# Kernel optimization log

Hardware: AMD Instinct MI355X
Metric: run time of the kernel (lower is better)

Reference implementation:

```python
import math
import jax, jax.numpy as jnp
import numpy as np

N = 100000
E_RAND = 800000
IN_F, HID, OUT_F, HEADS = 128, 64, 64, 4
NOISE_SCALE = 1.0 * math.sqrt(2.0 * math.log(1.25 / 0.05))  # dp_rate=1, eps=1, del=0.05


def setup_inputs() -> dict:
    key = jax.random.key(0)
    ks = jax.random.split(key, 12)
    x = jax.random.normal(ks[0], (N, IN_F), dtype=jnp.float32)
    src_r = jax.random.randint(ks[1], (E_RAND,), 0, N, dtype=jnp.int32)
    dst_r = jax.random.randint(ks[2], (E_RAND,), 0, N, dtype=jnp.int32)
    loops = jnp.arange(N, dtype=jnp.int32)  # add_self_loop
    src = jnp.concatenate([src_r, loops])
    dst = jnp.concatenate([dst_r, loops])
    # layer 0: GATConv(in=128, out=64, heads=4)
    s0 = 1.0 / math.sqrt(IN_F)
    W0 = jax.random.normal(ks[3], (IN_F, HEADS * HID), dtype=jnp.float32) * s0
    al0 = jax.random.normal(ks[4], (HEADS, HID), dtype=jnp.float32) * 0.1
    ar0 = jax.random.normal(ks[5], (HEADS, HID), dtype=jnp.float32) * 0.1
    b0 = jnp.zeros((HEADS * HID,), dtype=jnp.float32)
    # layer 1: GATConv(in=256, out=64, heads=1)
    s1 = 1.0 / math.sqrt(HEADS * HID)
    W1 = jax.random.normal(ks[6], (HEADS * HID, OUT_F), dtype=jnp.float32) * s1
    al1 = jax.random.normal(ks[7], (1, OUT_F), dtype=jnp.float32) * 0.1
    ar1 = jax.random.normal(ks[8], (1, OUT_F), dtype=jnp.float32) * 0.1
    b1 = jnp.zeros((OUT_F,), dtype=jnp.float32)
    # DP gaussian noise added after first GAT layer (torch.normal(0,1,x.shape))
    noise = jax.random.normal(ks[9], (N, HEADS * HID), dtype=jnp.float32)
    return {"x": x, "src": src, "dst": dst, "W0": W0, "al0": al0, "ar0": ar0,
            "b0": b0, "W1": W1, "al1": al1, "ar1": ar1, "b1": b1, "noise": noise}


def gat_conv(x, src, dst, W, al, ar, b, apply_act):
    """DGL GATConv: per-edge attention, edge softmax over dst, scatter-sum."""
    H, D = al.shape
    h = (x @ W).reshape(-1, H, D)                      # [N,H,D]
    el = jnp.sum(h * al, axis=-1)                      # [N,H]
    er = jnp.sum(h * ar, axis=-1)                      # [N,H]
    e = jax.nn.leaky_relu(el[src] + er[dst], 0.2)      # [E,H]
    emax = jax.ops.segment_max(e, dst, num_segments=N) # [N,H]
    a = jnp.exp(e - emax[dst])
    denom = jax.ops.segment_sum(a, dst, num_segments=N)
    alpha = a / denom[dst]                             # [E,H] edge softmax
    msg = h[src] * alpha[:, :, None]                   # [E,H,D]
    out = jax.ops.segment_sum(msg, dst, num_segments=N) + b.reshape(1, H, D)
    if apply_act:
        out = jax.nn.leaky_relu(out, 0.01)             # F.leaky_relu default slope
    return out.reshape(-1, H * D)                      # flatten(1)


def reference(x, src, dst, W0, al0, ar0, b0, W1, al1, ar1, b1, noise):
    h = gat_conv(x, src, dst, W0, al0, ar0, b0, apply_act=True)   # [N, 256]
    h = h + NOISE_SCALE * noise                                   # DP noise after layer 0
    out = gat_conv(h, src, dst, W1, al1, ar1, b1, apply_act=False)  # [N, 64]
    return out
```

## Files before the change

kernel.cpp:

```cpp
#include <hip/hip_runtime.h>
#include <hip/hip_bf16.h>
#include <math.h>

#define IN_F 128
#define HID 64
#define HEADS 4
#define HD0 (HEADS * HID)
#define OUT_F 64
#define NOISE_SCALE 2.5372725354060904f

typedef __bf16 bf16x8 __attribute__((ext_vector_type(8)));
typedef float f32x4 __attribute__((ext_vector_type(4)));

__device__ __forceinline__ float bf2f(unsigned short u) {
    return __uint_as_float(((unsigned)u) << 16);
}
__device__ __forceinline__ unsigned short f2bf(float f) {
    unsigned u = __float_as_uint(f);
    u = u + 0x7fffu + ((u >> 16) & 1u);
    return (unsigned short)(u >> 16);
}

__global__ __launch_bounds__(256) void cast_bf16_kernel(
    const float* __restrict__ in, unsigned short* __restrict__ out, size_t n8) {
    size_t i = (size_t)blockIdx.x * 256 + threadIdx.x;
    if (i >= n8) return;
    const float4 a = ((const float4*)in)[i * 2];
    const float4 b = ((const float4*)in)[i * 2 + 1];
    ushort4 o0, o1;
    o0.x = f2bf(a.x); o0.y = f2bf(a.y); o0.z = f2bf(a.z); o0.w = f2bf(a.w);
    o1.x = f2bf(b.x); o1.y = f2bf(b.y); o1.z = f2bf(b.z); o1.w = f2bf(b.w);
    ((ushort4*)out)[i * 2] = o0;
    ((ushort4*)out)[i * 2 + 1] = o1;
}

__global__ __launch_bounds__(256) void tcast_kernel(
    const float* __restrict__ W, unsigned short* __restrict__ Wt, int K, int NC) {
    int i = blockIdx.x * 256 + threadIdx.x;
    if (i >= K * NC) return;
    int n = i / K, k = i % K;
    Wt[n * K + k] = f2bf(W[(size_t)k * NC + n]);
}

template <int K, int H>
__global__ __launch_bounds__(256) void gemm_fused_kernel(
    const unsigned short* __restrict__ A, const unsigned short* __restrict__ Bt,
    unsigned short* __restrict__ C, const float* __restrict__ al,
    const float* __restrict__ ar, float* __restrict__ el,
    float* __restrict__ er, int M, int NC) {
    constexpr int BSTR = K + 8;
    constexpr int ASTR = 40;
    __shared__ __align__(16) unsigned short Bs[64 * BSTR];
    __shared__ __align__(16) unsigned short As[128 * ASTR];
    const int tid = threadIdx.x;
    const int lane = tid & 63, w = tid >> 6;
    const int row0 = blockIdx.y * 128;
    const int n0 = blockIdx.x * 64;
    for (int i = tid; i < 64 * (K / 8); i += 256) {
        int n = i / (K / 8), kc = i % (K / 8);
        *(uint4*)(Bs + n * BSTR + kc * 8) =
            *(const uint4*)(Bt + (size_t)(n0 + n) * K + kc * 8);
    }
    f32x4 acc[2][4] = {};
    const int q = lane >> 4, c = lane & 15;
    const int r_st = tid >> 1, hh = tid & 1;
    for (int k0 = 0; k0 < K; k0 += 32) {
        int gr = row0 + r_st;
        uint4 av0 = make_uint4(0, 0, 0, 0), av1 = make_uint4(0, 0, 0, 0);
        if (gr < M) {
            const unsigned short* ap = A + (size_t)gr * K + k0 + hh * 16;
            av0 = *(const uint4*)(ap);
            av1 = *(const uint4*)(ap + 8);
        }
        __syncthreads();
        *(uint4*)(As + r_st * ASTR + hh * 16) = av0;
        *(uint4*)(As + r_st * ASTR + hh * 16 + 8) = av1;
        __syncthreads();
        bf16x8 af[2], bfr[4];
        af[0] = *(const bf16x8*)(As + (w * 32 + c) * ASTR + q * 8);
        af[1] = *(const bf16x8*)(As + (w * 32 + 16 + c) * ASTR + q * 8);
#pragma unroll
        for (int nt = 0; nt < 4; ++nt)
            bfr[nt] = *(const bf16x8*)(Bs + (nt * 16 + c) * BSTR + k0 + q * 8);
#pragma unroll
        for (int mt = 0; mt < 2; ++mt)
#pragma unroll
            for (int nt = 0; nt < 4; ++nt)
                acc[mt][nt] = __builtin_amdgcn_mfma_f32_16x16x32_bf16(
                    af[mt], bfr[nt], acc[mt][nt], 0, 0, 0);
    }
    float alv[4], arv[4];
#pragma unroll
    for (int nt = 0; nt < 4; ++nt) {
        alv[nt] = al[n0 + nt * 16 + c];
        arv[nt] = ar[n0 + nt * 16 + c];
    }
    const int head = n0 >> 6;
#pragma unroll
    for (int mt = 0; mt < 2; ++mt) {
#pragma unroll
        for (int r = 0; r < 4; ++r) {
            int grow = row0 + w * 32 + mt * 16 + q * 4 + r;
            bool ok = grow < M;
            float elp = 0.f, erp = 0.f;
#pragma unroll
            for (int nt = 0; nt < 4; ++nt) {
                float v = acc[mt][nt][r];
                elp += v * alv[nt];
                erp += v * arv[nt];
                if (ok) C[(size_t)grow * NC + n0 + nt * 16 + c] = f2bf(v);
            }
#pragma unroll
            for (int o = 8; o > 0; o >>= 1) {
                elp += __shfl_down(elp, o, 16);
                erp += __shfl_down(erp, o, 16);
            }
            if (c == 0 && ok) {
                el[(size_t)grow * H + head] = elp;
                er[(size_t)grow * H + head] = erp;
            }
        }
    }
}

__global__ __launch_bounds__(256) void degree_kernel(
    const int* __restrict__ dst, int* __restrict__ deg, int E) {
    int e = blockIdx.x * 256 + threadIdx.x;
    if (e < E) atomicAdd(&deg[dst[e]], 1);
}

__global__ __launch_bounds__(256) void scan_block_kernel(
    const int* __restrict__ deg, int* __restrict__ off,
    int* __restrict__ bsum, int N) {
    __shared__ int s[256];
    int i = blockIdx.x * 256 + threadIdx.x;
    int v = (i < N) ? deg[i] : 0;
    s[threadIdx.x] = v;
    __syncthreads();
    for (int d = 1; d < 256; d <<= 1) {
        int t = (threadIdx.x >= d) ? s[threadIdx.x - d] : 0;
        __syncthreads();
        s[threadIdx.x] += t;
        __syncthreads();
    }
    if (i < N) off[i] = s[threadIdx.x] - v;
    if (threadIdx.x == 255) bsum[blockIdx.x] = s[255];
}

__global__ __launch_bounds__(512) void scan_partials_kernel(int* __restrict__ bsum, int nb) {
    __shared__ int s[512];
    int v = (threadIdx.x < nb) ? bsum[threadIdx.x] : 0;
    s[threadIdx.x] = v;
    __syncthreads();
    for (int d = 1; d < 512; d <<= 1) {
        int t = (threadIdx.x >= d) ? s[threadIdx.x - d] : 0;
        __syncthreads();
        s[threadIdx.x] += t;
        __syncthreads();
    }
    if (threadIdx.x < nb) bsum[threadIdx.x] = s[threadIdx.x] - v;
}

__global__ __launch_bounds__(256) void add_offsets_kernel(
    int* __restrict__ off, int* __restrict__ cur,
    const int* __restrict__ bsum, int N, int E) {
    int i = blockIdx.x * 256 + threadIdx.x;
    if (i < N) {
        int v = off[i] + bsum[blockIdx.x];
        off[i] = v;
        cur[i] = v;
    }
    if (i == 0) off[N] = E;
}

__global__ __launch_bounds__(256) void fill_csr_kernel(
    const int* __restrict__ src, const int* __restrict__ dst,
    int* __restrict__ cur, int* __restrict__ csr_src, int E) {
    int e = blockIdx.x * 256 + threadIdx.x;
    if (e >= E) return;
    int d = dst[e];
    int pos = atomicAdd(&cur[d], 1);
    csr_src[pos] = src[e];
}

__global__ __launch_bounds__(256) void agg0_kernel(
    const int* __restrict__ off, const int* __restrict__ csr_src,
    const unsigned short* __restrict__ h,
    const float* __restrict__ el,
    const float* __restrict__ er,
    const float* __restrict__ b0, const float* __restrict__ noise,
    unsigned short* __restrict__ out, int N) {
    int gt = blockIdx.x * 256 + threadIdx.x;
    int n = gt >> 6;
    int lane = gt & 63;
    if (n >= N) return;
    int hd = lane >> 4;
    float ern = er[(size_t)n * 4 + hd];
    int beg = off[n], end = off[n + 1];
    float ax = 0.f, ay = 0.f, az = 0.f, aw = 0.f, l = 0.f;
    int p = beg;
    for (; p + 4 <= end; p += 4) {
        int s0 = csr_src[p], s1 = csr_src[p + 1];
        int s2 = csr_src[p + 2], s3 = csr_src[p + 3];
        float e0 = el[(size_t)s0 * 4 + hd];
        float e1 = el[(size_t)s1 * 4 + hd];
        float e2 = el[(size_t)s2 * 4 + hd];
        float e3 = el[(size_t)s3 * 4 + hd];
        ushort4 u0 = *(const ushort4*)(h + (size_t)s0 * HD0 + lane * 4);
        ushort4 u1 = *(const ushort4*)(h + (size_t)s1 * HD0 + lane * 4);
        ushort4 u2 = *(const ushort4*)(h + (size_t)s2 * HD0 + lane * 4);
        ushort4 u3 = *(const ushort4*)(h + (size_t)s3 * HD0 + lane * 4);
        e0 += ern; e1 += ern; e2 += ern; e3 += ern;
        e0 = e0 > 0.f ? e0 : 0.2f * e0;
        e1 = e1 > 0.f ? e1 : 0.2f * e1;
        e2 = e2 > 0.f ? e2 : 0.2f * e2;
        e3 = e3 > 0.f ? e3 : 0.2f * e3;
        float w0 = __expf(e0), w1 = __expf(e1), w2 = __expf(e2), w3 = __expf(e3);
        ax += w0 * bf2f(u0.x) + w1 * bf2f(u1.x) + w2 * bf2f(u2.x) + w3 * bf2f(u3.x);
        ay += w0 * bf2f(u0.y) + w1 * bf2f(u1.y) + w2 * bf2f(u2.y) + w3 * bf2f(u3.y);
        az += w0 * bf2f(u0.z) + w1 * bf2f(u1.z) + w2 * bf2f(u2.z) + w3 * bf2f(u3.z);
        aw += w0 * bf2f(u0.w) + w1 * bf2f(u1.w) + w2 * bf2f(u2.w) + w3 * bf2f(u3.w);
        l += (w0 + w1) + (w2 + w3);
    }
    for (; p < end; ++p) {
        int s0 = csr_src[p];
        float e0 = el[(size_t)s0 * 4 + hd] + ern;
        e0 = e0 > 0.f ? e0 : 0.2f * e0;
        float w0 = __expf(e0);
        ushort4 u0 = *(const ushort4*)(h + (size_t)s0 * HD0 + lane * 4);
        ax += w0 * bf2f(u0.x);
        ay += w0 * bf2f(u0.y);
        az += w0 * bf2f(u0.z);
        aw += w0 * bf2f(u0.w);
        l += w0;
    }
    float rd = 1.f / l;
    const float4 bv = *(const float4*)(b0 + lane * 4);
    const float4 nv = *(const float4*)(noise + (size_t)n * HD0 + lane * 4);
    float ox = ax * rd + bv.x; ox = ox > 0.f ? ox : 0.01f * ox; ox += NOISE_SCALE * nv.x;
    float oy = ay * rd + bv.y; oy = oy > 0.f ? oy : 0.01f * oy; oy += NOISE_SCALE * nv.y;
    float oz = az * rd + bv.z; oz = oz > 0.f ? oz : 0.01f * oz; oz += NOISE_SCALE * nv.z;
    float ow = aw * rd + bv.w; ow = ow > 0.f ? ow : 0.01f * ow; ow += NOISE_SCALE * nv.w;
    ushort4 o;
    o.x = f2bf(ox); o.y = f2bf(oy); o.z = f2bf(oz); o.w = f2bf(ow);
    *(ushort4*)(out + (size_t)n * HD0 + lane * 4) = o;
}

__global__ __launch_bounds__(256) void agg1_kernel(
    const int* __restrict__ off, const int* __restrict__ csr_src,
    const unsigned short* __restrict__ h,
    const float* __restrict__ el,
    const float* __restrict__ er,
    const float* __restrict__ b1, float* __restrict__ out, int N) {
    int gt = blockIdx.x * 256 + threadIdx.x;
    int n = gt >> 6;
    int lane = gt & 63;
    if (n >= N) return;
    float ern = er[n];
    int beg = off[n], end = off[n + 1];
    float acc = 0.f, l = 0.f;
    int p = beg;
    for (; p + 4 <= end; p += 4) {
        int s0 = csr_src[p], s1 = csr_src[p + 1];
        int s2 = csr_src[p + 2], s3 = csr_src[p + 3];
        float e0 = el[s0], e1 = el[s1], e2 = el[s2], e3 = el[s3];
        float v0 = bf2f(h[(size_t)s0 * 64 + lane]);
        float v1 = bf2f(h[(size_t)s1 * 64 + lane]);
        float v2 = bf2f(h[(size_t)s2 * 64 + lane]);
        float v3 = bf2f(h[(size_t)s3 * 64 + lane]);
        e0 += ern; e1 += ern; e2 += ern; e3 += ern;
        e0 = e0 > 0.f ? e0 : 0.2f * e0;
        e1 = e1 > 0.f ? e1 : 0.2f * e1;
        e2 = e2 > 0.f ? e2 : 0.2f * e2;
        e3 = e3 > 0.f ? e3 : 0.2f * e3;
        float w0 = __expf(e0), w1 = __expf(e1), w2 = __expf(e2), w3 = __expf(e3);
        acc += w0 * v0 + w1 * v1 + w2 * v2 + w3 * v3;
        l += (w0 + w1) + (w2 + w3);
    }
    for (; p < end; ++p) {
        int s0 = csr_src[p];
        float e0 = el[s0] + ern;
        e0 = e0 > 0.f ? e0 : 0.2f * e0;
        float w0 = __expf(e0);
        acc += w0 * bf2f(h[(size_t)s0 * 64 + lane]);
        l += w0;
    }
    out[(size_t)n * 64 + lane] = acc / l + b1[lane];
}

extern "C" void kernel_launch(void* const* d_in, const int* in_sizes, int n_in,
                              void* d_out, int out_size, void* d_ws, size_t ws_size,
                              hipStream_t stream) {
    const float* x     = (const float*)d_in[0];
    const int*   src   = (const int*)d_in[1];
    const int*   dst   = (const int*)d_in[2];
    const float* W0    = (const float*)d_in[3];
    const float* al0   = (const float*)d_in[4];
    const float* ar0   = (const float*)d_in[5];
    const float* b0    = (const float*)d_in[6];
    const float* W1    = (const float*)d_in[7];
    const float* al1   = (const float*)d_in[8];
    const float* ar1   = (const float*)d_in[9];
    const float* b1    = (const float*)d_in[10];
    const float* noise = (const float*)d_in[11];

    const int N = in_sizes[0] / IN_F;
    const int E = in_sizes[1];
    const int NB = (N + 255) / 256;

    char* p = (char*)d_ws;
    unsigned short* x_bf   = (unsigned short*)p; p += (size_t)N * IN_F * 2;
    unsigned short* h0     = (unsigned short*)p; p += (size_t)N * HD0 * 2;
    unsigned short* agg0b  = (unsigned short*)p; p += (size_t)N * HD0 * 2;
    unsigned short* h1     = (unsigned short*)p; p += (size_t)N * OUT_F * 2;
    unsigned short* W0t    = (unsigned short*)p; p += (size_t)IN_F * HD0 * 2;
    unsigned short* W1t    = (unsigned short*)p; p += (size_t)HD0 * OUT_F * 2;
    float* el     = (float*)p; p += (size_t)N * HEADS * 4;
    float* er     = (float*)p; p += (size_t)N * HEADS * 4;
    int* deg    = (int*)p; p += (size_t)N * 4;
    int* cur    = (int*)p; p += (size_t)N * 4;
    int* off    = (int*)p; p += ((size_t)N + 4) * 4;
    int* bsum   = (int*)p; p += 512 * 4;
    int* csr_src= (int*)p; p += (size_t)E * 4;

    {
        size_t n8 = (size_t)N * IN_F / 8;
        cast_bf16_kernel<<<(unsigned)((n8 + 255) / 256), 256, 0, stream>>>(x, x_bf, n8);
    }
    tcast_kernel<<<(IN_F * HD0 + 255) / 256, 256, 0, stream>>>(W0, W0t, IN_F, HD0);
    tcast_kernel<<<(HD0 * OUT_F + 255) / 256, 256, 0, stream>>>(W1, W1t, HD0, OUT_F);

    hipMemsetAsync(deg, 0, (size_t)N * sizeof(int), stream);
    degree_kernel<<<(E + 255) / 256, 256, 0, stream>>>(dst, deg, E);
    scan_block_kernel<<<NB, 256, 0, stream>>>(deg, off, bsum, N);
    scan_partials_kernel<<<1, 512, 0, stream>>>(bsum, NB);
    add_offsets_kernel<<<NB, 256, 0, stream>>>(off, cur, bsum, N, E);
    fill_csr_kernel<<<(E + 255) / 256, 256, 0, stream>>>(src, dst, cur, csr_src, E);

    const int MB = (N + 127) / 128;

    {
        dim3 grid(HD0 / 64, MB);
        gemm_fused_kernel<IN_F, HEADS><<<grid, 256, 0, stream>>>(
            x_bf, W0t, h0, al0, ar0, el, er, N, HD0);
    }
    agg0_kernel<<<(N * 64 + 255) / 256, 256, 0, stream>>>(
        off, csr_src, h0, el, er, b0, noise, agg0b, N);

    {
        dim3 grid(OUT_F / 64, MB);
        gemm_fused_kernel<HD0, 1><<<grid, 256, 0, stream>>>(
            agg0b, W1t, h1, al1, ar1, el, er, N, OUT_F);
    }
    agg1_kernel<<<(N * 64 + 255) / 256, 256, 0, stream>>>(
        off, csr_src, h1, el, er, b1, (float*)d_out, N);
}
```

Measured before the change: 483.4 us.

## Widen per-lane gather vectors in aggregation kernels and fuse setup launches

```diff
diff --git a/kernel.cpp b/kernel.cpp
--- a/kernel.cpp
+++ b/kernel.cpp
@@ -21,9 +21,22 @@
     return (unsigned short)(u >> 16);
 }
 
+__device__ __forceinline__ void acc8(float* acc, const uint4& u, float wt) {
+    acc[0] += wt * __uint_as_float(u.x << 16);
+    acc[1] += wt * __uint_as_float(u.x & 0xffff0000u);
+    acc[2] += wt * __uint_as_float(u.y << 16);
+    acc[3] += wt * __uint_as_float(u.y & 0xffff0000u);
+    acc[4] += wt * __uint_as_float(u.z << 16);
+    acc[5] += wt * __uint_as_float(u.z & 0xffff0000u);
+    acc[6] += wt * __uint_as_float(u.w << 16);
+    acc[7] += wt * __uint_as_float(u.w & 0xffff0000u);
+}
+
 __global__ __launch_bounds__(256) void cast_bf16_kernel(
-    const float* __restrict__ in, unsigned short* __restrict__ out, size_t n8) {
+    const float* __restrict__ in, unsigned short* __restrict__ out, size_t n8,
+    int* __restrict__ deg, int N) {
     size_t i = (size_t)blockIdx.x * 256 + threadIdx.x;
+    if (i < (size_t)N) deg[i] = 0;
     if (i >= n8) return;
     const float4 a = ((const float4*)in)[i * 2];
     const float4 b = ((const float4*)in)[i * 2 + 1];
@@ -34,12 +47,20 @@
     ((ushort4*)out)[i * 2 + 1] = o1;
 }
 
-__global__ __launch_bounds__(256) void tcast_kernel(
-    const float* __restrict__ W, unsigned short* __restrict__ Wt, int K, int NC) {
+__global__ __launch_bounds__(256) void tcast2_kernel(
+    const float* __restrict__ W0, unsigned short* __restrict__ W0t,
+    const float* __restrict__ W1, unsigned short* __restrict__ W1t) {
     int i = blockIdx.x * 256 + threadIdx.x;
-    if (i >= K * NC) return;
-    int n = i / K, k = i % K;
-    Wt[n * K + k] = f2bf(W[(size_t)k * NC + n]);
+    if (i < IN_F * HD0) {
+        int n = i / IN_F, k = i % IN_F;
+        W0t[i] = f2bf(W0[(size_t)k * HD0 + n]);
+    } else {
+        int j = i - IN_F * HD0;
+        if (j < HD0 * OUT_F) {
+            int n = j / HD0, k = j % HD0;
+            W1t[j] = f2bf(W1[(size_t)k * OUT_F + n]);
+        }
+    }
 }
 
 template <int K, int H>
@@ -191,59 +212,76 @@
     const float* __restrict__ b0, const float* __restrict__ noise,
     unsigned short* __restrict__ out, int N) {
     int gt = blockIdx.x * 256 + threadIdx.x;
-    int n = gt >> 6;
-    int lane = gt & 63;
+    int n = gt >> 5;
     if (n >= N) return;
-    int hd = lane >> 4;
-    float ern = er[(size_t)n * 4 + hd];
-    int beg = off[n], end = off[n + 1];
-    float ax = 0.f, ay = 0.f, az = 0.f, aw = 0.f, l = 0.f;
-    int p = beg;
-    for (; p + 4 <= end; p += 4) {
-        int s0 = csr_src[p], s1 = csr_src[p + 1];
-        int s2 = csr_src[p + 2], s3 = csr_src[p + 3];
-        float e0 = el[(size_t)s0 * 4 + hd];
-        float e1 = el[(size_t)s1 * 4 + hd];
-        float e2 = el[(size_t)s2 * 4 + hd];
-        float e3 = el[(size_t)s3 * 4 + hd];
-        ushort4 u0 = *(const ushort4*)(h + (size_t)s0 * HD0 + lane * 4);
-        ushort4 u1 = *(const ushort4*)(h + (size_t)s1 * HD0 + lane * 4);
-        ushort4 u2 = *(const ushort4*)(h + (size_t)s2 * HD0 + lane * 4);
-        ushort4 u3 = *(const ushort4*)(h + (size_t)s3 * HD0 + lane * 4);
-        e0 += ern; e1 += ern; e2 += ern; e3 += ern;
+    const int lane = gt & 31;
+    const int hd = lane >> 3;
+    const int f0 = lane << 3;
+    const float ern = er[(size_t)n * 4 + hd];
+    const int beg = off[n];
+    const int last = off[n + 1] - 1;
+    float acc[8] = {0.f, 0.f, 0.f, 0.f, 0.f, 0.f, 0.f, 0.f};
+    float l = 0.f;
+    for (int p = beg; p <= last; p += 4) {
+        int i1 = p + 1, i2 = p + 2, i3 = p + 3;
+        const bool v1 = i1 <= last, v2 = i2 <= last, v3 = i3 <= last;
+        i1 = v1 ? i1 : last;
+        i2 = v2 ? i2 : last;
+        i3 = v3 ? i3 : last;
+        const int s0 = csr_src[p],  s1 = csr_src[i1];
+        const int s2 = csr_src[i2], s3 = csr_src[i3];
+        float e0 = el[(size_t)s0 * 4 + hd] + ern;
+        float e1 = el[(size_t)s1 * 4 + hd] + ern;
+        float e2 = el[(size_t)s2 * 4 + hd] + ern;
+        float e3 = el[(size_t)s3 * 4 + hd] + ern;
+        const uint4 u0 = *(const uint4*)(h + (size_t)s0 * HD0 + f0);
+        const uint4 u1 = *(const uint4*)(h + (size_t)s1 * HD0 + f0);
+        const uint4 u2 = *(const uint4*)(h + (size_t)s2 * HD0 + f0);
+        const uint4 u3 = *(const uint4*)(h + (size_t)s3 * HD0 + f0);
         e0 = e0 > 0.f ? e0 : 0.2f * e0;
         e1 = e1 > 0.f ? e1 : 0.2f * e1;
         e2 = e2 > 0.f ? e2 : 0.2f * e2;
         e3 = e3 > 0.f ? e3 : 0.2f * e3;
-        float w0 = __expf(e0), w1 = __expf(e1), w2 = __expf(e2), w3 = __expf(e3);
-        ax += w0 * bf2f(u0.x) + w1 * bf2f(u1.x) + w2 * bf2f(u2.x) + w3 * bf2f(u3.x);
-        ay += w0 * bf2f(u0.y) + w1 * bf2f(u1.y) + w2 * bf2f(u2.y) + w3 * bf2f(u3.y);
-        az += w0 * bf2f(u0.z) + w1 * bf2f(u1.z) + w2 * bf2f(u2.z) + w3 * bf2f(u3.z);
-        aw += w0 * bf2f(u0.w) + w1 * bf2f(u1.w) + w2 * bf2f(u2.w) + w3 * bf2f(u3.w);
+        const float w0 = __expf(e0);
+        const float w1 = v1 ? __expf(e1) : 0.f;
+        const float w2 = v2 ? __expf(e2) : 0.f;
+        const float w3 = v3 ? __expf(e3) : 0.f;
+        acc8(acc, u0, w0);
+        acc8(acc, u1, w1);
+        acc8(acc, u2, w2);
+        acc8(acc, u3, w3);
         l += (w0 + w1) + (w2 + w3);
     }
-    for (; p < end; ++p) {
-        int s0 = csr_src[p];
-        float e0 = el[(size_t)s0 * 4 + hd] + ern;
-        e0 = e0 > 0.f ? e0 : 0.2f * e0;
-        float w0 = __expf(e0);
-        ushort4 u0 = *(const ushort4*)(h + (size_t)s0 * HD0 + lane * 4);
-        ax += w0 * bf2f(u0.x);
-        ay += w0 * bf2f(u0.y);
-        az += w0 * bf2f(u0.z);
-        aw += w0 * bf2f(u0.w);
-        l += w0;
-    }
-    float rd = 1.f / l;
-    const float4 bv = *(const float4*)(b0 + lane * 4);
-    const float4 nv = *(const float4*)(noise + (size_t)n * HD0 + lane * 4);
-    float ox = ax * rd + bv.x; ox = ox > 0.f ? ox : 0.01f * ox; ox += NOISE_SCALE * nv.x;
-    float oy = ay * rd + bv.y; oy = oy > 0.f ? oy : 0.01f * oy; oy += NOISE_SCALE * nv.y;
-    float oz = az * rd + bv.z; oz = oz > 0.f ? oz : 0.01f * oz; oz += NOISE_SCALE * nv.z;
-    float ow = aw * rd + bv.w; ow = ow > 0.f ? ow : 0.01f * ow; ow += NOISE_SCALE * nv.w;
-    ushort4 o;
-    o.x = f2bf(ox); o.y = f2bf(oy); o.z = f2bf(oz); o.w = f2bf(ow);
-    *(ushort4*)(out + (size_t)n * HD0 + lane * 4) = o;
+    const float rd = 1.f / l;
+    const float4 ba = *(const float4*)(b0 + f0);
+    const float4 bb = *(const float4*)(b0 + f0 + 4);
+    const float4 na = *(const float4*)(noise + (size_t)n * HD0 + f0);
+    const float4 nb = *(const float4*)(noise + (size_t)n * HD0 + f0 + 4);
+    float o[8];
+    o[0] = acc[0] * rd + ba.x;
+    o[1] = acc[1] * rd + ba.y;
+    o[2] = acc[2] * rd + ba.z;
+    o[3] = acc[3] * rd + ba.w;
+    o[4] = acc[4] * rd + bb.x;
+    o[5] = acc[5] * rd + bb.y;
+    o[6] = acc[6] * rd + bb.z;
+    o[7] = acc[7] * rd + bb.w;
+#pragma unroll
+    for (int j = 0; j < 8; ++j) o[j] = o[j] > 0.f ? o[j] : 0.01f * o[j];
+    o[0] += NOISE_SCALE * na.x;
+    o[1] += NOISE_SCALE * na.y;
+    o[2] += NOISE_SCALE * na.z;
+    o[3] += NOISE_SCALE * na.w;
+    o[4] += NOISE_SCALE * nb.x;
+    o[5] += NOISE_SCALE * nb.y;
+    o[6] += NOISE_SCALE * nb.z;
+    o[7] += NOISE_SCALE * nb.w;
+    uint4 ov;
+    ov.x = (unsigned)f2bf(o[0]) | ((unsigned)f2bf(o[1]) << 16);
+    ov.y = (unsigned)f2bf(o[2]) | ((unsigned)f2bf(o[3]) << 16);
+    ov.z = (unsigned)f2bf(o[4]) | ((unsigned)f2bf(o[5]) << 16);
+    ov.w = (unsigned)f2bf(o[6]) | ((unsigned)f2bf(o[7]) << 16);
+    *(uint4*)(out + (size_t)n * HD0 + f0) = ov;
 }
 
 __global__ __launch_bounds__(256) void agg1_kernel(
@@ -253,39 +291,52 @@
     const float* __restrict__ er,
     const float* __restrict__ b1, float* __restrict__ out, int N) {
     int gt = blockIdx.x * 256 + threadIdx.x;
-    int n = gt >> 6;
-    int lane = gt & 63;
+    int n = gt >> 4;
     if (n >= N) return;
-    float ern = er[n];
-    int beg = off[n], end = off[n + 1];
-    float acc = 0.f, l = 0.f;
-    int p = beg;
-    for (; p + 4 <= end; p += 4) {
-        int s0 = csr_src[p], s1 = csr_src[p + 1];
-        int s2 = csr_src[p + 2], s3 = csr_src[p + 3];
-        float e0 = el[s0], e1 = el[s1], e2 = el[s2], e3 = el[s3];
-        float v0 = bf2f(h[(size_t)s0 * 64 + lane]);
-        float v1 = bf2f(h[(size_t)s1 * 64 + lane]);
-        float v2 = bf2f(h[(size_t)s2 * 64 + lane]);
-        float v3 = bf2f(h[(size_t)s3 * 64 + lane]);
-        e0 += ern; e1 += ern; e2 += ern; e3 += ern;
+    const int lane = gt & 15;
+    const int f0 = lane << 2;
+    const float ern = er[n];
+    const int beg = off[n];
+    const int last = off[n + 1] - 1;
+    float a0 = 0.f, a1 = 0.f, a2 = 0.f, a3 = 0.f, l = 0.f;
+    for (int p = beg; p <= last; p += 4) {
+        int i1 = p + 1, i2 = p + 2, i3 = p + 3;
+        const bool v1 = i1 <= last, v2 = i2 <= last, v3 = i3 <= last;
+        i1 = v1 ? i1 : last;
+        i2 = v2 ? i2 : last;
+        i3 = v3 ? i3 : last;
+        const int s0 = csr_src[p],  s1 = csr_src[i1];
+        const int s2 = csr_src[i2], s3 = csr_src[i3];
+        float e0 = el[s0] + ern;
+        float e1 = el[s1] + ern;
+        float e2 = el[s2] + ern;
+        float e3 = el[s3] + ern;
+        const ushort4 u0 = *(const ushort4*)(h + (size_t)s0 * 64 + f0);
+        const ushort4 u1 = *(const ushort4*)(h + (size_t)s1 * 64 + f0);
+        const ushort4 u2 = *(const ushort4*)(h + (size_t)s2 * 64 + f0);
+        const ushort4 u3 = *(const ushort4*)(h + (size_t)s3 * 64 + f0);
         e0 = e0 > 0.f ? e0 : 0.2f * e0;
         e1 = e1 > 0.f ? e1 : 0.2f * e1;
         e2 = e2 > 0.f ? e2 : 0.2f * e2;
         e3 = e3 > 0.f ? e3 : 0.2f * e3;
-        float w0 = __expf(e0), w1 = __expf(e1), w2 = __expf(e2), w3 = __expf(e3);
-        acc += w0 * v0 + w1 * v1 + w2 * v2 + w3 * v3;
+        const float w0 = __expf(e0);
+        const float w1 = v1 ? __expf(e1) : 0.f;
+        const float w2 = v2 ? __expf(e2) : 0.f;
+        const float w3 = v3 ? __expf(e3) : 0.f;
+        a0 += w0 * bf2f(u0.x) + w1 * bf2f(u1.x) + w2 * bf2f(u2.x) + w3 * bf2f(u3.x);
+        a1 += w0 * bf2f(u0.y) + w1 * bf2f(u1.y) + w2 * bf2f(u2.y) + w3 * bf2f(u3.y);
+        a2 += w0 * bf2f(u0.z) + w1 * bf2f(u1.z) + w2 * bf2f(u2.z) + w3 * bf2f(u3.z);
+        a3 += w0 * bf2f(u0.w) + w1 * bf2f(u1.w) + w2 * bf2f(u2.w) + w3 * bf2f(u3.w);
         l += (w0 + w1) + (w2 + w3);
     }
-    for (; p < end; ++p) {
-        int s0 = csr_src[p];
-        float e0 = el[s0] + ern;
-        e0 = e0 > 0.f ? e0 : 0.2f * e0;
-        float w0 = __expf(e0);
-        acc += w0 * bf2f(h[(size_t)s0 * 64 + lane]);
-        l += w0;
-    }
-    out[(size_t)n * 64 + lane] = acc / l + b1[lane];
+    const float rd = 1.f / l;
+    const float4 bv = *(const float4*)(b1 + f0);
+    float4 o;
+    o.x = a0 * rd + bv.x;
+    o.y = a1 * rd + bv.y;
+    o.z = a2 * rd + bv.z;
+    o.w = a3 * rd + bv.w;
+    *(float4*)(out + (size_t)n * 64 + f0) = o;
 }
 
 extern "C" void kernel_launch(void* const* d_in, const int* in_sizes, int n_in,
@@ -325,12 +376,12 @@
 
     {
         size_t n8 = (size_t)N * IN_F / 8;
-        cast_bf16_kernel<<<(unsigned)((n8 + 255) / 256), 256, 0, stream>>>(x, x_bf, n8);
-    }
-    tcast_kernel<<<(IN_F * HD0 + 255) / 256, 256, 0, stream>>>(W0, W0t, IN_F, HD0);
-    tcast_kernel<<<(HD0 * OUT_F + 255) / 256, 256, 0, stream>>>(W1, W1t, HD0, OUT_F);
-
-    hipMemsetAsync(deg, 0, (size_t)N * sizeof(int), stream);
+        cast_bf16_kernel<<<(unsigned)((n8 + 255) / 256), 256, 0, stream>>>(
+            x, x_bf, n8, deg, N);
+    }
+    tcast2_kernel<<<(IN_F * HD0 + HD0 * OUT_F + 255) / 256, 256, 0, stream>>>(
+        W0, W0t, W1, W1t);
+
     degree_kernel<<<(E + 255) / 256, 256, 0, stream>>>(dst, deg, E);
     scan_block_kernel<<<NB, 256, 0, stream>>>(deg, off, bsum, N);
     scan_partials_kernel<<<1, 512, 0, stream>>>(bsum, NB);
@@ -344,7 +395,7 @@
         gemm_fused_kernel<IN_F, HEADS><<<grid, 256, 0, stream>>>(
             x_bf, W0t, h0, al0, ar0, el, er, N, HD0);
     }
-    agg0_kernel<<<(N * 64 + 255) / 256, 256, 0, stream>>>(
+    agg0_kernel<<<(unsigned)(((size_t)N * 32 + 255) / 256), 256, 0, stream>>>(
         off, csr_src, h0, el, er, b0, noise, agg0b, N);
 
     {
@@ -352,6 +403,6 @@
         gemm_fused_kernel<HD0, 1><<<grid, 256, 0, stream>>>(
             agg0b, W1t, h1, al1, ar1, el, er, N, OUT_F);
     }
-    agg1_kernel<<<(N * 64 + 255) / 256, 256, 0, stream>>>(
+    agg1_kernel<<<(unsigned)(((size_t)N * 16 + 255) / 256), 256, 0, stream>>>(
         off, csr_src, h1, el, er, b1, (float*)d_out, N);
 }
```

After: 435.2 us. 1.11x faster.
